# Kernel optimization log

Hardware: AMD Instinct MI355X
Metric: run time of the kernel (lower is better)

The kernel has to match this reference:

```python
import jax, jax.numpy as jnp
import numpy as np

N_HEADS = 8
BUCKET = 64
EPS = 1e-4


def setup_inputs() -> dict:
    key = jax.random.key(0)
    ks = jax.random.split(key, 8)
    B, S, D = 4, 8192, 1024
    s = 1.0 / np.sqrt(D).astype(np.float32)
    x = jax.random.normal(ks[0], (B, S, D), dtype=jnp.float32)
    W_hash = jax.random.normal(ks[1], (D, 2 * N_HEADS), dtype=jnp.float32) * s
    W_q = jax.random.normal(ks[2], (D, D), dtype=jnp.float32) * s
    b_q = jax.random.normal(ks[3], (D,), dtype=jnp.float32) * 0.01
    W_v = jax.random.normal(ks[4], (D, D), dtype=jnp.float32) * s
    b_v = jax.random.normal(ks[5], (D,), dtype=jnp.float32) * 0.01
    W_o = jax.random.normal(ks[6], (D, D), dtype=jnp.float32) * s
    b_o = jax.random.normal(ks[7], (D,), dtype=jnp.float32) * 0.01
    return {"x": x, "W_hash": W_hash, "W_q": W_q, "b_q": b_q,
            "W_v": W_v, "b_v": b_v, "W_o": W_o, "b_o": b_o}


def reference(x, W_hash, W_q, b_q, W_v, b_v, W_o, b_o):
    B, S, D = x.shape
    H, dh = N_HEADS, D // N_HEADS
    nb = S // BUCKET  # number of LSH buckets per head

    # --- LSH hash: one angle per head, sort tokens by angle (per head) ---
    h = (x @ W_hash).reshape(B, S, H, 2)
    angles = h[..., 0] / (h[..., 1] + EPS)          # [B, S, H]
    idx = jnp.argsort(angles.transpose(0, 2, 1), axis=2)  # [B, H, S]

    # --- projections (shared_qk: k uses the same projection as q) ---
    q = x @ W_q + b_q
    k = q
    v = x @ W_v + b_v

    def to_heads(t):
        return t.reshape(B, S, H, dh).transpose(0, 2, 1, 3)  # [B, H, S, dh]

    qh, kh, vh = to_heads(q), to_heads(k), to_heads(v)

    gather = lambda t: jnp.take_along_axis(t, idx[..., None], axis=2)
    qs = gather(qh).reshape(B, H, nb, BUCKET, dh)
    ks = gather(kh).reshape(B, H, nb, BUCKET, dh)
    vs = gather(vh).reshape(B, H, nb, BUCKET, dh)

    # --- bucketed local attention ---
    scale = 1.0 / np.sqrt(dh).astype(np.float32)
    scores = jnp.einsum('bhnid,bhnjd->bhnij', qs, ks) * scale
    attn = jax.nn.softmax(scores, axis=-1)
    o = jnp.einsum('bhnij,bhnjd->bhnid', attn, vs).reshape(B, H, S, dh)

    # --- unsort back to original token order ---
    inv = jnp.argsort(idx, axis=2)                  # inverse permutation [B, H, S]
    o = jnp.take_along_axis(o, inv[..., None], axis=2)
    o = o.transpose(0, 2, 1, 3).reshape(B, S, D)
    return o @ W_o + b_o
```

## Files before the change

kernel.cpp:

```cpp
#include <hip/hip_runtime.h>

typedef unsigned short u16;
typedef unsigned long long u64;
using short8 = __attribute__((ext_vector_type(8))) short;
using u16x8  = __attribute__((ext_vector_type(8))) unsigned short;
using f32x4  = __attribute__((ext_vector_type(4))) float;

#define B_   4
#define S_   8192
#define D_   1024
#define H_   8
#define DH_  128
#define NB_  128
#define M_   (B_ * S_)

static __device__ __forceinline__ float bf2f(u16 u) {
  union { unsigned int i; float f; } v; v.i = ((unsigned int)u) << 16; return v.f;
}
static __device__ __forceinline__ u16 f2bf(float f) {
  unsigned int x = __float_as_uint(f);
  unsigned int r = (x + 0x7fffu + ((x >> 16) & 1u)) >> 16;
  return (u16)r;
}
static __device__ __forceinline__ f32x4 mfma16(short8 a, short8 b, f32x4 c) {
  return __builtin_amdgcn_mfma_f32_16x16x32_bf16(a, b, c, 0, 0, 0);
}
static __device__ __forceinline__ void gload16(const u16* g, u16* l) {
  __builtin_amdgcn_global_load_lds(
      (const __attribute__((address_space(1))) void*)g,
      (__attribute__((address_space(3))) void*)l, 16, 0, 0);
}

__global__ __launch_bounds__(256) void cvt_k(const float* __restrict__ src,
                                             u16* __restrict__ dst) {
  const size_t i = ((size_t)blockIdx.x * 256 + threadIdx.x) * 8;
  const f32x4 a = *(const f32x4*)(src + i);
  const f32x4 b = *(const f32x4*)(src + i + 4);
  u16x8 r;
  r[0] = f2bf(a[0]); r[1] = f2bf(a[1]); r[2] = f2bf(a[2]); r[3] = f2bf(a[3]);
  r[4] = f2bf(b[0]); r[5] = f2bf(b[1]); r[6] = f2bf(b[2]); r[7] = f2bf(b[3]);
  *(u16x8*)(dst + i) = r;
}

__global__ __launch_bounds__(256) void transpose_k(const float* __restrict__ src,
                                                   u16* __restrict__ dst) {
  __shared__ float tile[32][33];
  const int bx = blockIdx.x * 32, by = blockIdx.y * 32;
  const int tx = threadIdx.x, ty = threadIdx.y;
#pragma unroll
  for (int i = ty; i < 32; i += 8) tile[i][tx] = src[(size_t)(by + i) * D_ + bx + tx];
  __syncthreads();
#pragma unroll
  for (int i = ty; i < 32; i += 8) dst[(size_t)(bx + i) * D_ + by + tx] = f2bf(tile[tx][i]);
}

__global__ __launch_bounds__(128) void keys_k(const float* __restrict__ x,
                                              const float* __restrict__ Wh,
                                              u64* __restrict__ keys) {
  __shared__ float wsh[D_ * 16];
  const int tid = threadIdx.x;
  for (int i = tid; i < D_ * 16; i += 128) wsh[i] = Wh[i];
  __syncthreads();
  const int token = blockIdx.x * 128 + tid;
  const float* xr = x + (size_t)token * D_;
  f32x4 acc4[4];
#pragma unroll
  for (int i = 0; i < 4; i++) acc4[i] = 0.0f;
  for (int d0 = 0; d0 < D_; d0 += 4) {
    const f32x4 pk = *(const f32x4*)(xr + d0);
#pragma unroll
    for (int j = 0; j < 4; j++) {
      const float xv = pk[j];
      const f32x4* wr = (const f32x4*)&wsh[(d0 + j) * 16];
#pragma unroll
      for (int c4 = 0; c4 < 4; c4++) acc4[c4] += wr[c4] * xv;
    }
  }
  const int b = token >> 13, s = token & (S_ - 1);
#pragma unroll
  for (int h = 0; h < H_; h++) {
    const float num = acc4[h >> 1][(h & 1) * 2 + 0];
    const float den = acc4[h >> 1][(h & 1) * 2 + 1];
    const float ang = num / (den + 1e-4f);
    unsigned int ub = __float_as_uint(ang);
    ub = (ub & 0x80000000u) ? ~ub : (ub | 0x80000000u);
    keys[(size_t)(b * H_ + h) * S_ + s] = ((u64)ub << 32) | (unsigned int)s;
  }
}


__global__ __launch_bounds__(1024) void sortA_k(u64* __restrict__ keys) {
  __shared__ u64 ks[2048];
  const int seq = blockIdx.y, chunk = blockIdx.x, t = threadIdx.x;
  u64* g = keys + ((size_t)seq << 13) + (chunk << 11);
  ks[t] = g[t]; ks[t + 1024] = g[t + 1024];
  __syncthreads();
  const int gbase = chunk << 11;
  for (int k = 2; k <= 2048; k <<= 1) {
    for (int j = k >> 1; j > 0; j >>= 1) {
      const int i = ((t & ~(j - 1)) << 1) | (t & (j - 1));
      const int p = i | j;
      const bool up = ((gbase + i) & k) == 0;
      const u64 a = ks[i], b = ks[p];
      if ((a > b) == up) { ks[i] = b; ks[p] = a; }
      __syncthreads();
    }
  }
  g[t] = ks[t]; g[t + 1024] = ks[t + 1024];
}

__global__ __launch_bounds__(256) void sortG_k(u64* __restrict__ keys, int j, int k) {
  const int p = blockIdx.x * 256 + threadIdx.x;
  const int seq = p >> 12, q = p & 4095;
  const int i = ((q & ~(j - 1)) << 1) | (q & (j - 1));
  u64* g = keys + ((size_t)seq << 13);
  const bool up = ((i & k) == 0);
  const u64 a = g[i], b = g[i | j];
  if ((a > b) == up) { g[i] = b; g[i | j] = a; }
}

template <int K, bool FINAL>
__global__ __launch_bounds__(1024) void sortB_k(u64* __restrict__ keys,
                                                int* __restrict__ idx) {
  __shared__ u64 ks[2048];
  const int seq = blockIdx.y, chunk = blockIdx.x, t = threadIdx.x;
  u64* g = keys + ((size_t)seq << 13) + (chunk << 11);
  ks[t] = g[t]; ks[t + 1024] = g[t + 1024];
  __syncthreads();
  const int gbase = chunk << 11;
#pragma unroll
  for (int j = 1024; j > 0; j >>= 1) {
    const int i = ((t & ~(j - 1)) << 1) | (t & (j - 1));
    const int p = i | j;
    const bool up = ((gbase + i) & K) == 0;
    const u64 a = ks[i], b = ks[p];
    if ((a > b) == up) { ks[i] = b; ks[p] = a; }
    __syncthreads();
  }
  if (FINAL) {
    int* o = idx + ((size_t)seq << 13) + (chunk << 11);
    o[t] = (int)(unsigned int)ks[t];
    o[t + 1024] = (int)(unsigned int)ks[t + 1024];
  } else {
    g[t] = ks[t]; g[t + 1024] = ks[t + 1024];
  }
}

template <bool CF32>
__global__ __launch_bounds__(256) void gemm_bt(const u16* __restrict__ A,
                                               const u16* __restrict__ Bt,
                                               const float* __restrict__ bias,
                                               void* __restrict__ Cv,
                                               int M, int N, int K) {
  __shared__ __attribute__((aligned(16))) u16 As[128][32];
  __shared__ __attribute__((aligned(16))) u16 Bs[128][32];
  const int tid = threadIdx.x;
  const int wave = tid >> 6, lane = tid & 63;
  const int l16 = lane & 15, quad = lane >> 4;
  const int m0 = blockIdx.x * 128, n0 = blockIdx.y * 128;
  const int wm = wave >> 1, wn = wave & 1;
  const int srow = lane >> 2;
  const int scol = (lane & 3) * 8;

  const u16* Ag0 = A  + (size_t)(m0 + wave * 16 + srow) * K + scol;
  const u16* Ag1 = A  + (size_t)(m0 + 64 + wave * 16 + srow) * K + scol;
  const u16* Bg0 = Bt + (size_t)(n0 + wave * 16 + srow) * K + scol;
  const u16* Bg1 = Bt + (size_t)(n0 + 64 + wave * 16 + srow) * K + scol;
  u16* AsD0 = &As[wave * 16 + srow][scol];
  u16* AsD1 = &As[64 + wave * 16 + srow][scol];
  u16* BsD0 = &Bs[wave * 16 + srow][scol];
  u16* BsD1 = &Bs[64 + wave * 16 + srow][scol];

  f32x4 acc[4][4];
#pragma unroll
  for (int i = 0; i < 4; i++)
#pragma unroll
    for (int j = 0; j < 4; j++) acc[i][j] = 0.0f;

  for (int k0 = 0; k0 < K; k0 += 32) {
    __syncthreads();
    gload16(Ag0 + k0, AsD0);
    gload16(Ag1 + k0, AsD1);
    gload16(Bg0 + k0, BsD0);
    gload16(Bg1 + k0, BsD1);
    __syncthreads();
    short8 af[4], bfr[4];
#pragma unroll
    for (int i = 0; i < 4; i++)
      af[i] = *(const short8*)&As[wm * 64 + i * 16 + l16][quad * 8];
#pragma unroll
    for (int i = 0; i < 4; i++)
      bfr[i] = *(const short8*)&Bs[wn * 64 + i * 16 + l16][quad * 8];
#pragma unroll
    for (int mi = 0; mi < 4; mi++)
#pragma unroll
      for (int ni = 0; ni < 4; ni++)
        acc[mi][ni] = mfma16(af[mi], bfr[ni], acc[mi][ni]);
  }

#pragma unroll
  for (int ni = 0; ni < 4; ni++) {
    const int col = n0 + wn * 64 + ni * 16 + l16;
    const float bv = bias[col];
#pragma unroll
    for (int mi = 0; mi < 4; mi++) {
      const int rowb = m0 + wm * 64 + mi * 16 + quad * 4;
#pragma unroll
      for (int r = 0; r < 4; r++) {
        const float cv = acc[mi][ni][r] + bv;
        if (CF32) ((float*)Cv)[(size_t)(rowb + r) * N + col] = cv;
        else      ((u16*)Cv)[(size_t)(rowb + r) * N + col] = f2bf(cv);
      }
    }
  }
}

__global__ __launch_bounds__(256) void attn_k(const u16* __restrict__ qbuf,
                                              const u16* __restrict__ vbuf,
                                              const int* __restrict__ idx,
                                              u16* __restrict__ obuf) {
  __shared__ u16  Qs[64][136];
  __shared__ u16  Vt[128][72];
  __shared__ float Ss[64][65];
  __shared__ u16  Ps[64][72];
  __shared__ int  tids[64];
  const int b = blockIdx.z, h = blockIdx.y, n = blockIdx.x;
  const int tid = threadIdx.x;
  const int lane = tid & 63, wave = tid >> 6;
  const int l16 = lane & 15, quad = lane >> 4;

  if (tid < 64) tids[tid] = idx[(size_t)(b * H_ + h) * S_ + n * 64 + tid];
  __syncthreads();

  {
    const int i = tid & 63, seg = tid >> 6;
    const size_t rowoff = (size_t)(b * S_ + tids[i]) * D_ + h * DH_ + seg * 32;
    const u16* qr = qbuf + rowoff;
    const u16* vr = vbuf + rowoff;
#pragma unroll
    for (int c = 0; c < 32; c += 8)
      *(u16x8*)&Qs[i][seg * 32 + c] = *(const u16x8*)(qr + c);
#pragma unroll
    for (int c = 0; c < 32; c += 8) {
      u16x8 pv = *(const u16x8*)(vr + c);
#pragma unroll
      for (int j = 0; j < 8; j++) Vt[seg * 32 + c + j][i] = pv[j];
    }
  }
  __syncthreads();

  f32x4 sacc[4];
#pragma unroll
  for (int i = 0; i < 4; i++) sacc[i] = 0.0f;
#pragma unroll
  for (int k0 = 0; k0 < DH_; k0 += 32) {
    const short8 af = *(const short8*)&Qs[wave * 16 + l16][k0 + quad * 8];
#pragma unroll
    for (int ni = 0; ni < 4; ni++) {
      const short8 bfr = *(const short8*)&Qs[ni * 16 + l16][k0 + quad * 8];
      sacc[ni] = mfma16(af, bfr, sacc[ni]);
    }
  }
  const float scale = 0.08838834764831845f;
#pragma unroll
  for (int ni = 0; ni < 4; ni++)
#pragma unroll
    for (int r = 0; r < 4; r++)
      Ss[wave * 16 + quad * 4 + r][ni * 16 + l16] = sacc[ni][r] * scale;
  __syncthreads();

  {
    const int row = tid >> 2, part = tid & 3;
    float e[16]; float mx = -3.0e38f;
#pragma unroll
    for (int c = 0; c < 16; c++) { e[c] = Ss[row][part * 16 + c]; mx = fmaxf(mx, e[c]); }
    mx = fmaxf(mx, __shfl_xor(mx, 1));
    mx = fmaxf(mx, __shfl_xor(mx, 2));
    float sum = 0.f;
#pragma unroll
    for (int c = 0; c < 16; c++) { e[c] = __expf(e[c] - mx); sum += e[c]; }
    sum += __shfl_xor(sum, 1);
    sum += __shfl_xor(sum, 2);
    const float inv = 1.0f / sum;
#pragma unroll
    for (int c = 0; c < 16; c++) Ps[row][part * 16 + c] = f2bf(e[c] * inv);
  }
  __syncthreads();

  f32x4 oacc[8];
#pragma unroll
  for (int i = 0; i < 8; i++) oacc[i] = 0.0f;
#pragma unroll
  for (int k0 = 0; k0 < 64; k0 += 32) {
    const short8 pf = *(const short8*)&Ps[wave * 16 + l16][k0 + quad * 8];
#pragma unroll
    for (int nt = 0; nt < 8; nt++) {
      const short8 vf = *(const short8*)&Vt[nt * 16 + l16][k0 + quad * 8];
      oacc[nt] = mfma16(pf, vf, oacc[nt]);
    }
  }

  u16 (*Os)[128] = (u16(*)[128])&Ss[0][0];
#pragma unroll
  for (int r = 0; r < 4; r++) {
    const int m = wave * 16 + quad * 4 + r;
    const int swz = ((m >> 2) & 3) * 32;
#pragma unroll
    for (int nt = 0; nt < 8; nt++) Os[m][(nt * 16 + l16) ^ swz] = f2bf(oacc[nt][r]);
  }
  __syncthreads();

  {
    const int row = tid >> 2, c0 = (tid & 3) * 32;
    const int swz = ((row >> 2) & 3) * 32;
    u16* orow = obuf + (size_t)(b * S_ + tids[row]) * D_ + h * DH_ + c0;
#pragma unroll
    for (int c = 0; c < 32; c += 8)
      *(u16x8*)(orow + c) = *(const u16x8*)&Os[row][(c0 + c) ^ swz];
  }
}

extern "C" void kernel_launch(void* const* d_in, const int* in_sizes, int n_in,
                              void* d_out, int out_size, void* d_ws, size_t ws_size,
                              hipStream_t stream) {
  const float* x  = (const float*)d_in[0];
  const float* Wh = (const float*)d_in[1];
  const float* Wq = (const float*)d_in[2];
  const float* bq = (const float*)d_in[3];
  const float* Wv = (const float*)d_in[4];
  const float* bv = (const float*)d_in[5];
  const float* Wo = (const float*)d_in[6];
  const float* bo = (const float*)d_in[7];
  char* ws = (char*)d_ws;
  u16*   Wqt    = (u16*)(ws);
  u16*   Wvt    = (u16*)(ws + (2u << 20));
  u16*   Wot    = (u16*)(ws + (4u << 20));
  int*   idxb   = (int*)(ws + (7u << 20));
  u16*   qbuf   = (u16*)(ws + (8u << 20));
  u16*   xbf    = (u16*)d_out;
  u16*   vbuf   = (u16*)((char*)d_out + (64u << 20));
  u64*   keys   = (u64*)((char*)d_out + (64u << 20));
  float* out    = (float*)d_out;

  cvt_k<<<dim3(M_ * D_ / (256 * 8), 1, 1), dim3(256, 1, 1), 0, stream>>>(x, xbf);
  transpose_k<<<dim3(32, 32, 1), dim3(32, 8, 1), 0, stream>>>(Wq, Wqt);
  transpose_k<<<dim3(32, 32, 1), dim3(32, 8, 1), 0, stream>>>(Wv, Wvt);
  transpose_k<<<dim3(32, 32, 1), dim3(32, 8, 1), 0, stream>>>(Wo, Wot);
  keys_k<<<dim3(M_ / 128, 1, 1), dim3(128, 1, 1), 0, stream>>>(x, Wh, keys);
  sortA_k<<<dim3(4, 32, 1), dim3(1024, 1, 1), 0, stream>>>(keys);
  sortG_k<<<dim3(512, 1, 1), dim3(256, 1, 1), 0, stream>>>(keys, 2048, 4096);
  sortB_k<4096, false><<<dim3(4, 32, 1), dim3(1024, 1, 1), 0, stream>>>(keys, idxb);
  sortG_k<<<dim3(512, 1, 1), dim3(256, 1, 1), 0, stream>>>(keys, 4096, 8192);
  sortG_k<<<dim3(512, 1, 1), dim3(256, 1, 1), 0, stream>>>(keys, 2048, 8192);
  sortB_k<8192, true><<<dim3(4, 32, 1), dim3(1024, 1, 1), 0, stream>>>(keys, idxb);
  gemm_bt<false><<<dim3(M_ / 128, D_ / 128, 1), dim3(256, 1, 1), 0, stream>>>(xbf, Wqt, bq, qbuf, M_, D_, D_);
  gemm_bt<false><<<dim3(M_ / 128, D_ / 128, 1), dim3(256, 1, 1), 0, stream>>>(xbf, Wvt, bv, vbuf, M_, D_, D_);
  attn_k<<<dim3(NB_, H_, B_), dim3(256, 1, 1), 0, stream>>>(qbuf, vbuf, idxb, qbuf);
  gemm_bt<true><<<dim3(M_ / 128, D_ / 128, 1), dim3(256, 1, 1), 0, stream>>>(qbuf, Wot, bo, out, M_, D_, D_);
}
```

Baseline: 708.4 us.

## Enlarge GEMM tiles to 256x256 with 64-wide K, XOR-swizzled LDS, staged bf16 stores

The projection GEMM now uses 256x256 output tiles with 512 threads and a K step of 64. Each wave computes a 128x64 sub-tile, and LDS is addressed with an XOR swizzle to avoid bank conflicts. For bf16 output the results are staged through LDS and written back as coalesced 16-byte stores. The goal is more data reuse per global load, fewer barriers per K, and better store coalescing. The cost is 64KB of LDS per block and more accumulator registers, which may limit occupancy.

```diff
diff --git a/kernel.cpp b/kernel.cpp
--- a/kernel.cpp
+++ b/kernel.cpp
@@ -88,7 +88,6 @@
   }
 }
 
-
 __global__ __launch_bounds__(1024) void sortA_k(u64* __restrict__ keys) {
   __shared__ u64 ks[2048];
   const int seq = blockIdx.y, chunk = blockIdx.x, t = threadIdx.x;
@@ -147,70 +146,103 @@
 }
 
 template <bool CF32>
-__global__ __launch_bounds__(256) void gemm_bt(const u16* __restrict__ A,
-                                               const u16* __restrict__ Bt,
-                                               const float* __restrict__ bias,
-                                               void* __restrict__ Cv,
-                                               int M, int N, int K) {
-  __shared__ __attribute__((aligned(16))) u16 As[128][32];
-  __shared__ __attribute__((aligned(16))) u16 Bs[128][32];
+__global__ __launch_bounds__(512, 2) void gemm_bt(const u16* __restrict__ A,
+                                                  const u16* __restrict__ Bt,
+                                                  const float* __restrict__ bias,
+                                                  void* __restrict__ Cv,
+                                                  int M, int N, int K) {
+  __shared__ __attribute__((aligned(16))) u16 lds[65536];
   const int tid = threadIdx.x;
   const int wave = tid >> 6, lane = tid & 63;
   const int l16 = lane & 15, quad = lane >> 4;
-  const int m0 = blockIdx.x * 128, n0 = blockIdx.y * 128;
-  const int wm = wave >> 1, wn = wave & 1;
-  const int srow = lane >> 2;
-  const int scol = (lane & 3) * 8;
-
-  const u16* Ag0 = A  + (size_t)(m0 + wave * 16 + srow) * K + scol;
-  const u16* Ag1 = A  + (size_t)(m0 + 64 + wave * 16 + srow) * K + scol;
-  const u16* Bg0 = Bt + (size_t)(n0 + wave * 16 + srow) * K + scol;
-  const u16* Bg1 = Bt + (size_t)(n0 + 64 + wave * 16 + srow) * K + scol;
-  u16* AsD0 = &As[wave * 16 + srow][scol];
-  u16* AsD1 = &As[64 + wave * 16 + srow][scol];
-  u16* BsD0 = &Bs[wave * 16 + srow][scol];
-  u16* BsD1 = &Bs[64 + wave * 16 + srow][scol];
-
-  f32x4 acc[4][4];
-#pragma unroll
-  for (int i = 0; i < 4; i++)
+  const int wm = wave >> 2, wn = wave & 3;
+  const int m0 = blockIdx.x * 256, n0 = blockIdx.y * 256;
+
+  const int rl = tid >> 3, ss = tid & 7;
+  const int scol = ((ss ^ (rl & 7)) << 3);
+  const u16* Ag = A  + (size_t)(m0 + rl) * K + scol;
+  const u16* Bg = Bt + (size_t)(n0 + rl) * K + scol;
+
+  f32x4 acc[8][4];
+#pragma unroll
+  for (int i = 0; i < 8; i++)
 #pragma unroll
     for (int j = 0; j < 4; j++) acc[i][j] = 0.0f;
 
-  for (int k0 = 0; k0 < K; k0 += 32) {
+  const int NT = K >> 6;
+  for (int t = 0; t < NT; ++t) {
     __syncthreads();
-    gload16(Ag0 + k0, AsD0);
-    gload16(Ag1 + k0, AsD1);
-    gload16(Bg0 + k0, BsD0);
-    gload16(Bg1 + k0, BsD1);
+    {
+      const size_t k0s = (size_t)t * 64;
+      u16* ad = lds + tid * 8;
+      u16* bd = lds + 16384 + tid * 8;
+#pragma unroll
+      for (int j = 0; j < 4; ++j) {
+        gload16(Ag + (size_t)(64 * j) * K + k0s, ad + j * 4096);
+        gload16(Bg + (size_t)(64 * j) * K + k0s, bd + j * 4096);
+      }
+    }
     __syncthreads();
-    short8 af[4], bfr[4];
-#pragma unroll
-    for (int i = 0; i < 4; i++)
-      af[i] = *(const short8*)&As[wm * 64 + i * 16 + l16][quad * 8];
-#pragma unroll
-    for (int i = 0; i < 4; i++)
-      bfr[i] = *(const short8*)&Bs[wn * 64 + i * 16 + l16][quad * 8];
-#pragma unroll
-    for (int mi = 0; mi < 4; mi++)
-#pragma unroll
-      for (int ni = 0; ni < 4; ni++)
-        acc[mi][ni] = mfma16(af[mi], bfr[ni], acc[mi][ni]);
-  }
-
-#pragma unroll
-  for (int ni = 0; ni < 4; ni++) {
-    const int col = n0 + wn * 64 + ni * 16 + l16;
-    const float bv = bias[col];
-#pragma unroll
-    for (int mi = 0; mi < 4; mi++) {
-      const int rowb = m0 + wm * 64 + mi * 16 + quad * 4;
-#pragma unroll
-      for (int r = 0; r < 4; r++) {
-        const float cv = acc[mi][ni][r] + bv;
-        if (CF32) ((float*)Cv)[(size_t)(rowb + r) * N + col] = cv;
-        else      ((u16*)Cv)[(size_t)(rowb + r) * N + col] = f2bf(cv);
-      }
+    const u16* Ab = lds;
+    const u16* Bb = lds + 16384;
+#pragma unroll
+    for (int kh = 0; kh < 2; ++kh) {
+      short8 a[8], b[4];
+#pragma unroll
+      for (int mi = 0; mi < 8; ++mi) {
+        const int r = wm * 128 + mi * 16 + l16;
+        a[mi] = *(const short8*)(Ab + r * 64 + (((kh * 4 + quad) ^ (r & 7)) << 3));
+      }
+#pragma unroll
+      for (int ni = 0; ni < 4; ++ni) {
+        const int r = wn * 64 + ni * 16 + l16;
+        b[ni] = *(const short8*)(Bb + r * 64 + (((kh * 4 + quad) ^ (r & 7)) << 3));
+      }
+#pragma unroll
+      for (int mi = 0; mi < 8; ++mi)
+#pragma unroll
+        for (int ni = 0; ni < 4; ++ni)
+          acc[mi][ni] = mfma16(a[mi], b[ni], acc[mi][ni]);
+    }
+  }
+  __syncthreads();
+
+  if (CF32) {
+#pragma unroll
+    for (int ni = 0; ni < 4; ++ni) {
+      const int col = n0 + wn * 64 + ni * 16 + l16;
+      const float bv = bias[col];
+#pragma unroll
+      for (int mi = 0; mi < 8; ++mi) {
+        const int rowb = m0 + wm * 128 + mi * 16 + quad * 4;
+#pragma unroll
+        for (int r = 0; r < 4; ++r)
+          ((float*)Cv)[(size_t)(rowb + r) * N + col] = acc[mi][ni][r] + bv;
+      }
+    }
+  } else {
+    u16* Cs = lds;
+#pragma unroll
+    for (int ni = 0; ni < 4; ++ni) {
+      const int col = wn * 64 + ni * 16 + l16;
+      const float bv = bias[n0 + col];
+#pragma unroll
+      for (int mi = 0; mi < 8; ++mi) {
+#pragma unroll
+        for (int r = 0; r < 4; ++r) {
+          const int row = wm * 128 + mi * 16 + quad * 4 + r;
+          Cs[row * 256 + col] = f2bf(acc[mi][ni][r] + bv);
+        }
+      }
+    }
+    __syncthreads();
+    u16* Cg = (u16*)Cv;
+    const int rrow = tid >> 5, sl = tid & 31;
+#pragma unroll
+    for (int pass = 0; pass < 16; ++pass) {
+      const int row = pass * 16 + rrow;
+      *(u16x8*)(Cg + (size_t)(m0 + row) * N + n0 + sl * 8) =
+          *(const u16x8*)(Cs + row * 256 + sl * 8);
     }
   }
 }
@@ -353,8 +385,8 @@
   sortG_k<<<dim3(512, 1, 1), dim3(256, 1, 1), 0, stream>>>(keys, 4096, 8192);
   sortG_k<<<dim3(512, 1, 1), dim3(256, 1, 1), 0, stream>>>(keys, 2048, 8192);
   sortB_k<8192, true><<<dim3(4, 32, 1), dim3(1024, 1, 1), 0, stream>>>(keys, idxb);
-  gemm_bt<false><<<dim3(M_ / 128, D_ / 128, 1), dim3(256, 1, 1), 0, stream>>>(xbf, Wqt, bq, qbuf, M_, D_, D_);
-  gemm_bt<false><<<dim3(M_ / 128, D_ / 128, 1), dim3(256, 1, 1), 0, stream>>>(xbf, Wvt, bv, vbuf, M_, D_, D_);
+  gemm_bt<false><<<dim3(M_ / 256, D_ / 256, 1), dim3(512, 1, 1), 0, stream>>>(xbf, Wqt, bq, qbuf, M_, D_, D_);
+  gemm_bt<false><<<dim3(M_ / 256, D_ / 256, 1), dim3(512, 1, 1), 0, stream>>>(xbf, Wvt, bv, vbuf, M_, D_, D_);
   attn_k<<<dim3(NB_, H_, B_), dim3(256, 1, 1), 0, stream>>>(qbuf, vbuf, idxb, qbuf);
-  gemm_bt<true><<<dim3(M_ / 128, D_ / 128, 1), dim3(256, 1, 1), 0, stream>>>(qbuf, Wot, bo, out, M_, D_, D_);
-}
+  gemm_bt<true><<<dim3(M_ / 256, D_ / 256, 1), dim3(512, 1, 1), 0, stream>>>(qbuf, Wot, bo, out, M_, D_, D_);
+}
```

New measurement: 675.9 us. 1.05x faster.
